# Kernel optimization log

Measured on AMD Instinct MI355X. Metric: run time of the kernel, lower is better.

The kernel has to match this reference:

```python
import jax, jax.numpy as jnp
import numpy as np

B, S, HIDDEN, H, KVH, D = 4, 1024, 4096, 32, 8, 128
ROT = D // 2  # rotary_dim = head_size/2 (inv_freq over arange(0, dim, 2))
NUM_SLOTS = 8192
ROPE_THETA = 10000.0


def setup_inputs() -> dict:
    key = jax.random.key(0)
    k0, k1, k2 = jax.random.split(key, 3)
    T = B * S
    hidden_states = jax.random.normal(k0, (T, HIDDEN), dtype=jnp.float32) * 0.02
    # RoPE tables: positions 0..S-1 per sequence, gathered per token, shape [T,1,ROT]
    inv_freq = 1.0 / (ROPE_THETA ** (np.arange(0, D, 2, dtype=np.float32) / D))
    pos = jnp.tile(jnp.arange(S, dtype=jnp.float32), B)          # [T]
    freqs = pos[:, None] * jnp.asarray(inv_freq)[None, :]        # [T, ROT]
    cos = jnp.cos(freqs)[:, None, :]
    sin = jnp.sin(freqs)[:, None, :]
    w_qkv = jax.random.normal(k1, (H * D + 2 * KVH * D, HIDDEN), dtype=jnp.float32) * 0.02
    w_o = jax.random.normal(k2, (HIDDEN, H * D), dtype=jnp.float32) * 0.02
    slots = jnp.arange(T, dtype=jnp.int32)
    key_cache = jnp.zeros((NUM_SLOTS, KVH, D), dtype=jnp.float32)
    value_cache = jnp.zeros((NUM_SLOTS, KVH, D), dtype=jnp.float32)
    return {"hidden_states": hidden_states, "cos": cos, "sin": sin,
            "w_qkv": w_qkv, "w_o": w_o,
            "key_cache": key_cache, "value_cache": value_cache,
            "slots": slots, "seq_len": S}


def _rope(x, cos, sin):
    # x: [T, heads, D]; cos/sin: [T, 1, ROT]; NeoX half-split rotation
    x1, x2 = x[..., :ROT], x[..., ROT:2 * ROT]
    return jnp.concatenate([x1 * cos - x2 * sin, x1 * sin + x2 * cos], axis=-1)


def reference(hidden_states, cos, sin, w_qkv, w_o, key_cache, value_cache, slots, seq_len):
    T, hidden = hidden_states.shape
    kvh = key_cache.shape[1]
    d = key_cache.shape[2]
    h = (w_qkv.shape[0] - 2 * kvh * d) // d
    b = T // seq_len
    groups = h // kvh
    scale = d ** -0.5

    # fused QKV projection
    qkv = hidden_states @ w_qkv.T                              # [T, (h+2*kvh)*d]
    q = qkv[:, : h * d].reshape(T, h, d)
    k = qkv[:, h * d: h * d + kvh * d].reshape(T, kvh, d)
    v = qkv[:, h * d + kvh * d:].reshape(T, kvh, d)

    # in-place RoPE on query and key
    q = _rope(q, cos, sin)
    k = _rope(k, cos, sin)

    # reshape_and_cache: scatter rotated K and V into slot-indexed cache
    new_key_cache = key_cache.at[slots].set(k)
    new_value_cache = value_cache.at[slots].set(v)

    # prefill varlen flash attention (equal-length sequences), causal, GQA
    qb = q.reshape(b, seq_len, h, d)
    kb = jnp.repeat(k.reshape(b, seq_len, kvh, d), groups, axis=2)  # [b,s,h,d]
    vb = jnp.repeat(v.reshape(b, seq_len, kvh, d), groups, axis=2)
    scores = jnp.einsum('bqhd,bkhd->bhqk', qb, kb) * scale
    causal = jnp.tril(jnp.ones((seq_len, seq_len), dtype=bool))
    scores = jnp.where(causal[None, None], scores, jnp.finfo(scores.dtype).min)
    attn = jax.nn.softmax(scores, axis=-1)
    out = jnp.einsum('bhqk,bkhd->bqhd', attn, vb).reshape(T, h * d)

    return out @ w_o.T, new_key_cache, new_value_cache
```

## Files before the change

kernel.cpp:

```cpp
#include <hip/hip_runtime.h>
#include <hip/hip_bf16.h>

#define B_    4
#define S_    1024
#define HID   4096
#define H_    32
#define KVH_  8
#define D_    128
#define T_    (B_ * S_)
#define QKVD  (H_ * D_ + 2 * KVH_ * D_)
#define NSLOT 8192

typedef __attribute__((ext_vector_type(8))) short short8;
typedef __attribute__((ext_vector_type(4))) float f32x4;

#define MFMA_B16(d, x, y) \
  d = __builtin_amdgcn_mfma_f32_16x16x32_bf16(x, y, d, 0, 0, 0)

__device__ __forceinline__ unsigned short f2b(float f) {
  union { __hip_bfloat16 h; unsigned short u; } c;
  c.h = __float2bfloat16(f);
  return c.u;
}
__device__ __forceinline__ float b2f(unsigned short u) {
  union { unsigned int i; float f; } c;
  c.i = ((unsigned int)u) << 16;
  return c.f;
}

__device__ __forceinline__ void async16(const void* g, void* l) {
  __builtin_amdgcn_global_load_lds(
      (const __attribute__((address_space(1))) unsigned int*)g,
      (__attribute__((address_space(3))) unsigned int*)l,
      16, 0, 0);
}

__global__ void conv_bf16(const float* __restrict__ src,
                          unsigned short* __restrict__ dst, int n4) {
  int i = blockIdx.x * 256 + threadIdx.x;
  if (i >= n4) return;
  float4 v = reinterpret_cast<const float4*>(src)[i];
  ushort4 o;
  o.x = f2b(v.x); o.y = f2b(v.y); o.z = f2b(v.z); o.w = f2b(v.w);
  reinterpret_cast<ushort4*>(dst)[i] = o;
}

template <bool BF16OUT>
__global__ __launch_bounds__(512, 2) void gemm_bt(
    const unsigned short* __restrict__ A, const unsigned short* __restrict__ Bm,
    void* __restrict__ Cv, int M, int N, int K) {
  __shared__ unsigned short As[2 * 2 * 128 * 64];
  __shared__ unsigned short Bs[2 * 2 * 128 * 64];
  const int tid  = threadIdx.x;
  const int lane = tid & 63;
  const int w    = tid >> 6;
  const int quad = lane >> 4;
  const int l16  = lane & 15;
  const int bm = blockIdx.y * 256;
  const int bn = blockIdx.x * 256;
  const int wmh = w >> 2;
  const int wn  = (w & 3) * 64;
  const int hB  = (w & 3) >> 1;

  const int rr  = tid >> 3;
  const int gch = ((tid & 7) ^ (rr & 7)) * 8;
  const unsigned short* gA = A + (size_t)(bm + rr) * K + gch;
  const unsigned short* gB = Bm + (size_t)(bn + rr) * K + gch;
  const size_t r64 = (size_t)64 * K;

  const int cp0 = ((quad) ^ (l16 & 7)) * 8;
  const int cp1 = ((4 + quad) ^ (l16 & 7)) * 8;
  const int abase = wmh * 8192 + l16 * 64;
  const int bbase = hB * 8192 + ((w & 1) * 64 + l16) * 64;

  f32x4 acc[8][4];
#pragma unroll
  for (int f = 0; f < 8; f++)
#pragma unroll
    for (int c = 0; c < 4; c++)
#pragma unroll
      for (int r = 0; r < 4; r++) acc[f][c][r] = 0.f;

  auto stageA = [&](int tau, int h, int buf) {
    const unsigned short* s = gA + (size_t)(h * 2) * r64 + (size_t)tau * 64;
    unsigned short* d = As + buf * 16384 + h * 8192 + tid * 8;
    async16(s, d);
    async16(s + r64, d + 4096);
  };
  auto stageB = [&](int tau, int h, int buf) {
    const unsigned short* s = gB + (size_t)(h * 2) * r64 + (size_t)tau * 64;
    unsigned short* d = Bs + buf * 16384 + h * 8192 + tid * 8;
    async16(s, d);
    async16(s + r64, d + 4096);
  };

  stageA(0, 0, 0);
  stageA(0, 1, 0);
  stageB(0, 0, 0);
  stageB(0, 1, 0);
  stageA(1, 0, 1);
  asm volatile("s_waitcnt vmcnt(2)" ::: "memory");
  __builtin_amdgcn_s_barrier();

  const int KT = K >> 6;
  short8 a[4][2], b[4][2];
  for (int t = 0; t < KT; ++t) {
    const int cb = t & 1, nb = cb ^ 1;
    const int tn1 = (t + 1 < KT) ? t + 1 : KT - 1;
    const int tn2 = (t + 2 < KT) ? t + 2 : KT - 1;
    const unsigned short* Ab = As + cb * 16384 + abase;
    const unsigned short* Bb = Bs + cb * 16384 + bbase;

#pragma unroll
    for (int f = 0; f < 4; f++) {
      a[f][0] = *(const short8*)(Ab + f * 1024 + cp0);
      a[f][1] = *(const short8*)(Ab + f * 1024 + cp1);
    }
    b[0][0] = *(const short8*)(Bb + cp0);
    b[0][1] = *(const short8*)(Bb + cp1);
    b[1][0] = *(const short8*)(Bb + 1024 + cp0);
    b[1][1] = *(const short8*)(Bb + 1024 + cp1);
    stageA(tn1, 1, nb);
    __builtin_amdgcn_s_barrier();
    __builtin_amdgcn_s_setprio(1);
#pragma unroll
    for (int f = 0; f < 4; f++) {
      MFMA_B16(acc[f][0], a[f][0], b[0][0]);
      MFMA_B16(acc[f][0], a[f][1], b[0][1]);
      MFMA_B16(acc[f][1], a[f][0], b[1][0]);
      MFMA_B16(acc[f][1], a[f][1], b[1][1]);
    }
    __builtin_amdgcn_s_setprio(0);
    __builtin_amdgcn_s_barrier();

    b[2][0] = *(const short8*)(Bb + 2048 + cp0);
    b[2][1] = *(const short8*)(Bb + 2048 + cp1);
    b[3][0] = *(const short8*)(Bb + 3072 + cp0);
    b[3][1] = *(const short8*)(Bb + 3072 + cp1);
    stageB(tn1, 0, nb);
    __builtin_amdgcn_s_barrier();
    __builtin_amdgcn_s_setprio(1);
#pragma unroll
    for (int f = 0; f < 4; f++) {
      MFMA_B16(acc[f][2], a[f][0], b[2][0]);
      MFMA_B16(acc[f][2], a[f][1], b[2][1]);
      MFMA_B16(acc[f][3], a[f][0], b[3][0]);
      MFMA_B16(acc[f][3], a[f][1], b[3][1]);
    }
    __builtin_amdgcn_s_setprio(0);
    __builtin_amdgcn_s_barrier();

#pragma unroll
    for (int f = 0; f < 4; f++) {
      a[f][0] = *(const short8*)(Ab + 4096 + f * 1024 + cp0);
      a[f][1] = *(const short8*)(Ab + 4096 + f * 1024 + cp1);
    }
    stageB(tn1, 1, nb);
    __builtin_amdgcn_s_barrier();
    __builtin_amdgcn_s_setprio(1);
#pragma unroll
    for (int f = 0; f < 4; f++) {
      MFMA_B16(acc[4 + f][0], a[f][0], b[0][0]);
      MFMA_B16(acc[4 + f][0], a[f][1], b[0][1]);
      MFMA_B16(acc[4 + f][1], a[f][0], b[1][0]);
      MFMA_B16(acc[4 + f][1], a[f][1], b[1][1]);
    }
    __builtin_amdgcn_s_setprio(0);
    __builtin_amdgcn_s_barrier();

    stageA(tn2, 0, cb);
    asm volatile("s_waitcnt vmcnt(2)" ::: "memory");
    __builtin_amdgcn_s_barrier();
    __builtin_amdgcn_s_setprio(1);
#pragma unroll
    for (int f = 0; f < 4; f++) {
      MFMA_B16(acc[4 + f][2], a[f][0], b[2][0]);
      MFMA_B16(acc[4 + f][2], a[f][1], b[2][1]);
      MFMA_B16(acc[4 + f][3], a[f][0], b[3][0]);
      MFMA_B16(acc[4 + f][3], a[f][1], b[3][1]);
    }
    __builtin_amdgcn_s_setprio(0);
    __builtin_amdgcn_s_barrier();
  }
  asm volatile("s_waitcnt vmcnt(0)" ::: "memory");

  const int crow0 = bm + wmh * 128 + quad * 4;
  const int ccol0 = bn + wn + l16;
  if constexpr (BF16OUT) {
    unsigned short* C = (unsigned short*)Cv;
#pragma unroll
    for (int f = 0; f < 8; f++)
#pragma unroll
      for (int c = 0; c < 4; c++)
#pragma unroll
        for (int r = 0; r < 4; r++)
          C[(size_t)(crow0 + f * 16 + r) * N + ccol0 + c * 16] = f2b(acc[f][c][r]);
  } else {
    float* C = (float*)Cv;
#pragma unroll
    for (int f = 0; f < 8; f++)
#pragma unroll
      for (int c = 0; c < 4; c++)
#pragma unroll
        for (int r = 0; r < 4; r++)
          C[(size_t)(crow0 + f * 16 + r) * N + ccol0 + c * 16] = acc[f][c][r];
  }
}

__global__ void rope_scatter(
    const unsigned short* __restrict__ qkv, const float* __restrict__ cosb,
    const float* __restrict__ sinb, const int* __restrict__ slots,
    unsigned short* __restrict__ qb, unsigned short* __restrict__ kb,
    unsigned short* __restrict__ vb, float* __restrict__ kco,
    float* __restrict__ vco) {
  const float sl2 = 0.08838834764831843f * 1.4426950408889634f;
  const int t = blockIdx.x;
  const int tid = threadIdx.x;
  const int b = t >> 10, s = t & 1023;
  const unsigned short* row = qkv + (size_t)t * QKVD;
  const float* cs = cosb + (size_t)t * 64;
  const float* sn = sinb + (size_t)t * 64;
  const int slot = slots[t];
  for (int wk = tid; wk < H_ * 64; wk += 256) {
    int hh = wk >> 6, i = wk & 63;
    float x1 = b2f(row[hh * D_ + i]), x2 = b2f(row[hh * D_ + 64 + i]);
    float c = cs[i], sv = sn[i];
    size_t base = ((size_t)(b * H_ + hh) * S_ + s) * D_;
    qb[base + i]      = f2b((x1 * c - x2 * sv) * sl2);
    qb[base + 64 + i] = f2b((x1 * sv + x2 * c) * sl2);
  }
  for (int wk = tid; wk < KVH_ * 64; wk += 256) {
    int hh = wk >> 6, i = wk & 63;
    float x1 = b2f(row[H_ * D_ + hh * D_ + i]);
    float x2 = b2f(row[H_ * D_ + hh * D_ + 64 + i]);
    float c = cs[i], sv = sn[i];
    float o1 = x1 * c - x2 * sv, o2 = x1 * sv + x2 * c;
    size_t base = ((size_t)(b * KVH_ + hh) * S_ + s) * D_;
    kb[base + i] = f2b(o1);
    kb[base + 64 + i] = f2b(o2);
    size_t cb = ((size_t)slot * KVH_ + hh) * D_;
    kco[cb + i] = o1;
    kco[cb + 64 + i] = o2;
  }
  for (int wk = tid; wk < KVH_ * D_; wk += 256) {
    int hh = wk >> 7, i = wk & 127;
    unsigned short xv = row[H_ * D_ + KVH_ * D_ + hh * D_ + i];
    vb[((size_t)(b * KVH_ + hh) * S_ + s) * D_ + i] = xv;
    vco[((size_t)slot * KVH_ + hh) * D_ + i] = b2f(xv);
  }
}

__global__ void transpose_v(const unsigned short* __restrict__ vb,
                            unsigned short* __restrict__ vt) {
  __shared__ unsigned short tile[64][65];
  const int bid = blockIdx.x;
  const int dt = bid & 1, st = (bid >> 1) & 15, bk = bid >> 5;
  const int tid = threadIdx.x;
  const unsigned short* src = vb + ((size_t)bk * S_ + st * 64) * D_ + dt * 64;
#pragma unroll
  for (int k = 0; k < 16; k++) {
    int e = k * 256 + tid, r = e >> 6, c = e & 63;
    tile[r][c] = src[(size_t)r * D_ + c];
  }
  __syncthreads();
  unsigned short* dst = vt + ((size_t)bk * D_ + dt * 64) * S_ + st * 64;
#pragma unroll
  for (int k = 0; k < 16; k++) {
    int e = k * 256 + tid, r = e >> 6, c = e & 63;
    dst[(size_t)r * S_ + c] = tile[c][r];
  }
}

__global__ __launch_bounds__(256) void attn_fused(
    const unsigned short* __restrict__ qb, const unsigned short* __restrict__ kb,
    const unsigned short* __restrict__ vt, unsigned short* __restrict__ ob) {
  __shared__ unsigned short Ks[4 * 64 * 32];
  __shared__ unsigned short Vs[2 * 128 * 32];
  __shared__ unsigned short Ps[4][2 * 16 * 32];
  const int tid = threadIdx.x;
  const int lane = tid & 63, w = tid >> 6;
  const int quad = lane >> 4, l16 = lane & 15;
  const int bidx = blockIdx.x;
  const int qt = 15 - (bidx & 15);
  const int bh = bidx >> 4;
  const int h = bh & 31, b = bh >> 5;
  const int kvh = h >> 2;
  const int q0 = qt * 64;
  const unsigned short* qbase = qb + ((size_t)bh * S_ + q0) * D_;
  const unsigned short* kbase = kb + (size_t)(b * KVH_ + kvh) * S_ * D_;
  const unsigned short* vbase = vt + (size_t)(b * KVH_ + kvh) * D_ * S_;

  const int srow = tid >> 2;
  const int scol = (((tid & 3) ^ ((tid >> 3) & 3)) * 8);
  const int qoff = (quad ^ ((l16 >> 1) & 3)) * 8;

#pragma unroll
  for (int i = 0; i < 4; i++)
    async16(qbase + (size_t)srow * D_ + i * 32 + scol, (unsigned short*)Ks + i * 2048 + tid * 8);
  __syncthreads();
  short8 qf[4];
#pragma unroll
  for (int kc = 0; kc < 4; kc++)
    qf[kc] = *(const short8*)(Ks + (kc * 64 + w * 16 + l16) * 32 + qoff);

  short8 of;
  {
    unsigned short ov = (l16 == 0) ? (unsigned short)0x3F80 : (unsigned short)0;
#pragma unroll
    for (int j = 0; j < 8; j++) of[j] = (short)ov;
  }

  f32x4 oac[8];
  f32x4 osum;
#pragma unroll
  for (int n = 0; n < 8; n++)
#pragma unroll
    for (int r = 0; r < 4; r++) oac[n][r] = 0.f;
#pragma unroll
  for (int r = 0; r < 4; r++) osum[r] = 0.f;
  float m_run[4] = {-3.0e38f, -3.0e38f, -3.0e38f, -3.0e38f};

  unsigned short* psw = &Ps[w][0];
  const int qrow = q0 + w * 16 + quad * 4;

  for (int jt = 0; jt <= qt; jt++) {
    __syncthreads();
    const int j0 = jt * 64;
#pragma unroll
    for (int i = 0; i < 4; i++)
      async16(kbase + (size_t)(j0 + srow) * D_ + i * 32 + scol,
              (unsigned short*)Ks + i * 2048 + tid * 8);
#pragma unroll
    for (int i = 0; i < 4; i++) {
      int kc = i >> 1;
      int d = (i & 1) * 64 + srow;
      async16(vbase + (size_t)d * S_ + j0 + kc * 32 + scol,
              (unsigned short*)Vs + i * 2048 + tid * 8);
    }
    __syncthreads();

    f32x4 sac[4];
#pragma unroll
    for (int t = 0; t < 4; t++)
#pragma unroll
      for (int r = 0; r < 4; r++) sac[t][r] = 0.f;
#pragma unroll
    for (int t = 0; t < 4; t++)
#pragma unroll
      for (int kc = 0; kc < 4; kc++)
        sac[t] = __builtin_amdgcn_mfma_f32_16x16x32_bf16(
            qf[kc], *(const short8*)(Ks + (kc * 64 + t * 16 + l16) * 32 + qoff),
            sac[t], 0, 0, 0);

    if (jt == qt) {
#pragma unroll
      for (int t = 0; t < 4; t++) {
        const int kcol = j0 + t * 16 + l16;
#pragma unroll
        for (int r = 0; r < 4; r++)
          if (kcol > qrow + r) sac[t][r] = -3.0e38f;
      }
    }
    float mx[4];
#pragma unroll
    for (int r = 0; r < 4; r++)
      mx[r] = fmaxf(fmaxf(sac[0][r], sac[1][r]), fmaxf(sac[2][r], sac[3][r]));
#pragma unroll
    for (int off = 1; off < 16; off <<= 1)
#pragma unroll
      for (int r = 0; r < 4; r++) mx[r] = fmaxf(mx[r], __shfl_xor(mx[r], off));
    float alpha[4];
#pragma unroll
    for (int r = 0; r < 4; r++) {
      float mn = fmaxf(m_run[r], mx[r]);
      alpha[r] = exp2f(m_run[r] - mn);
      m_run[r] = mn;
    }
#pragma unroll
    for (int t = 0; t < 4; t++)
#pragma unroll
      for (int r = 0; r < 4; r++) {
        float p = exp2f(sac[t][r] - m_run[r]);
        int prow = quad * 4 + r;
        int chunk = (((t & 1) * 2 + (l16 >> 3)) ^ ((prow >> 1) & 3));
        psw[(t >> 1) * 512 + prow * 32 + chunk * 8 + (l16 & 7)] = f2b(p);
      }
#pragma unroll
    for (int r = 0; r < 4; r++) osum[r] *= alpha[r];
#pragma unroll
    for (int n = 0; n < 8; n++)
#pragma unroll
      for (int r = 0; r < 4; r++) oac[n][r] *= alpha[r];
#pragma unroll
    for (int kc = 0; kc < 2; kc++) {
      short8 pf = *(const short8*)(psw + kc * 512 + l16 * 32 + qoff);
      osum = __builtin_amdgcn_mfma_f32_16x16x32_bf16(pf, of, osum, 0, 0, 0);
#pragma unroll
      for (int n = 0; n < 8; n++)
        oac[n] = __builtin_amdgcn_mfma_f32_16x16x32_bf16(
            pf, *(const short8*)(Vs + (kc * 128 + n * 16 + l16) * 32 + qoff),
            oac[n], 0, 0, 0);
    }
  }

  float inv[4];
#pragma unroll
  for (int r = 0; r < 4; r++) {
    float l = __shfl(osum[r], lane & 48, 64);
    inv[r] = 1.0f / l;
  }
  const size_t trow = (size_t)(b * S_ + q0 + w * 16 + quad * 4);
#pragma unroll
  for (int n = 0; n < 8; n++)
#pragma unroll
    for (int r = 0; r < 4; r++)
      ob[(trow + r) * (size_t)(H_ * D_) + h * D_ + n * 16 + l16] =
          f2b(oac[n][r] * inv[r]);
}

extern "C" void kernel_launch(void* const* d_in, const int* in_sizes, int n_in,
                              void* d_out, int out_size, void* d_ws, size_t ws_size,
                              hipStream_t stream) {
  const float* hidden = (const float*)d_in[0];
  const float* cosb   = (const float*)d_in[1];
  const float* sinb   = (const float*)d_in[2];
  const float* wqkv   = (const float*)d_in[3];
  const float* wo     = (const float*)d_in[4];
  const float* kc_in  = (const float*)d_in[5];
  const float* vc_in  = (const float*)d_in[6];
  const int*   slots  = (const int*)d_in[7];

  float* out    = (float*)d_out;
  float* kc_out = out + (size_t)T_ * HID;
  float* vc_out = kc_out + (size_t)NSLOT * KVH_ * D_;

  char* ws = (char*)d_ws;
  unsigned short* hb    = (unsigned short*)ws; ws += (size_t)T_ * HID * 2;
  unsigned short* wqkvb = (unsigned short*)ws; ws += (size_t)QKVD * HID * 2;
  unsigned short* wob   = (unsigned short*)ws; ws += (size_t)HID * HID * 2;
  unsigned short* qkv   = (unsigned short*)ws; ws += (size_t)T_ * QKVD * 2;
  unsigned short* qb    = (unsigned short*)ws; ws += (size_t)T_ * H_ * D_ * 2;
  unsigned short* kb    = (unsigned short*)ws; ws += (size_t)T_ * KVH_ * D_ * 2;
  unsigned short* vb    = (unsigned short*)ws; ws += (size_t)T_ * KVH_ * D_ * 2;
  unsigned short* vt    = (unsigned short*)ws; ws += (size_t)T_ * KVH_ * D_ * 2;
  unsigned short* ob    = (unsigned short*)ws;

  const size_t cache_bytes = (size_t)NSLOT * KVH_ * D_ * 4;
  hipMemcpyAsync(kc_out, kc_in, cache_bytes, hipMemcpyDeviceToDevice, stream);
  hipMemcpyAsync(vc_out, vc_in, cache_bytes, hipMemcpyDeviceToDevice, stream);

  conv_bf16<<<(T_ * HID / 4) / 256, 256, 0, stream>>>(hidden, hb, T_ * HID / 4);
  conv_bf16<<<(QKVD * HID / 4) / 256, 256, 0, stream>>>(wqkv, wqkvb, QKVD * HID / 4);
  conv_bf16<<<(HID * HID / 4) / 256, 256, 0, stream>>>(wo, wob, HID * HID / 4);

  dim3 g1(QKVD / 256, T_ / 256);
  gemm_bt<true><<<g1, 512, 0, stream>>>(hb, wqkvb, qkv, T_, QKVD, HID);

  rope_scatter<<<T_, 256, 0, stream>>>(qkv, cosb, sinb, slots, qb, kb, vb, kc_out, vc_out);

  transpose_v<<<B_ * KVH_ * 16 * 2, 256, 0, stream>>>(vb, vt);

  attn_fused<<<B_ * H_ * (S_ / 64), 256, 0, stream>>>(qb, kb, vt, ob);

  dim3 g2(HID / 256, T_ / 256);
  gemm_bt<false><<<g2, 512, 0, stream>>>(ob, wob, out, T_, HID, HID);
}
```

Before: 918.4 us.

## Add a 256x192-tile QKV GEMM kernel to balance the grid across CUs

Adds a dedicated bf16 GEMM kernel for the QKV projection with 256x192 output tiles in place of 256x256. With N=6144 this gives 512 blocks, matching two resident blocks on each of 256 CUs, where the old tiling gave 384 blocks and left slots idle. The kernel has its own double-buffered async LDS pipeline with interleaved MFMA phases and priority hints. The trade-off is less operand reuse per tile, and the epilogue still writes scalar bf16 values with strided addresses.

```diff
diff --git a/kernel.cpp b/kernel.cpp
--- a/kernel.cpp
+++ b/kernel.cpp
@@ -43,6 +43,162 @@
   ushort4 o;
   o.x = f2b(v.x); o.y = f2b(v.y); o.z = f2b(v.z); o.w = f2b(v.w);
   reinterpret_cast<ushort4*>(dst)[i] = o;
+}
+
+__global__ __launch_bounds__(512, 2) void gemm1_192(
+    const unsigned short* __restrict__ A, const unsigned short* __restrict__ Bm,
+    unsigned short* __restrict__ C, int M, int N, int K) {
+  __shared__ unsigned short As[2 * 16384];
+  __shared__ unsigned short Bs[2 * 12288];
+  const int tid  = threadIdx.x;
+  const int lane = tid & 63;
+  const int w    = tid >> 6;
+  const int quad = lane >> 4;
+  const int l16  = lane & 15;
+  const int bm = blockIdx.y * 256;
+  const int bn = blockIdx.x * 192;
+  const int wmh = w >> 2;
+  const int wn  = (w & 3) * 48;
+
+  const int rr  = tid >> 3;
+  const int gch = ((tid & 7) ^ (rr & 7)) * 8;
+  const unsigned short* gA = A + (size_t)(bm + rr) * K + gch;
+  const unsigned short* gB = Bm + (size_t)(bn + rr) * K + gch;
+  const size_t r64 = (size_t)64 * K;
+
+  const int cp0 = ((quad) ^ (l16 & 7)) * 8;
+  const int cp1 = ((4 + quad) ^ (l16 & 7)) * 8;
+  const int abase = wmh * 8192 + l16 * 64;
+  const int bbase = (wn + l16) * 64;
+
+  f32x4 acc[8][3];
+#pragma unroll
+  for (int f = 0; f < 8; f++)
+#pragma unroll
+    for (int c = 0; c < 3; c++)
+#pragma unroll
+      for (int r = 0; r < 4; r++) acc[f][c][r] = 0.f;
+
+  auto stA = [&](int tau, int h, int buf) {
+    const unsigned short* s = gA + (size_t)(h * 2) * r64 + (size_t)tau * 64;
+    unsigned short* d = As + buf * 16384 + h * 8192 + tid * 8;
+    async16(s, d);
+    async16(s + r64, d + 4096);
+  };
+  auto stB = [&](int tau, int g, int buf) {
+    const unsigned short* s = gB + (size_t)g * r64 + (size_t)tau * 64;
+    unsigned short* d = Bs + buf * 12288 + g * 4096 + tid * 8;
+    async16(s, d);
+  };
+
+  stA(0, 0, 0);
+  stA(0, 1, 0);
+  stB(0, 0, 0); stB(0, 1, 0); stB(0, 2, 0);
+  stA(1, 0, 1);
+  asm volatile("s_waitcnt vmcnt(2)" ::: "memory");
+  __builtin_amdgcn_s_barrier();
+
+  short8 aA[4][2], aB[4][2], b[3][2];
+  {
+    const unsigned short* Ab = As + abase;
+    const unsigned short* Bb = Bs + bbase;
+#pragma unroll
+    for (int f = 0; f < 4; f++) {
+      aA[f][0] = *(const short8*)(Ab + f * 1024 + cp0);
+      aA[f][1] = *(const short8*)(Ab + f * 1024 + cp1);
+    }
+    b[0][0] = *(const short8*)(Bb + cp0);
+    b[0][1] = *(const short8*)(Bb + cp1);
+    b[1][0] = *(const short8*)(Bb + 1024 + cp0);
+    b[1][1] = *(const short8*)(Bb + 1024 + cp1);
+  }
+
+  const int KT = K >> 6;
+  for (int t = 0; t < KT; ++t) {
+    const int cb = t & 1, nb = cb ^ 1;
+    const int tn1 = (t + 1 < KT) ? t + 1 : KT - 1;
+    const int tn2 = (t + 2 < KT) ? t + 2 : KT - 1;
+    const unsigned short* Ab  = As + cb * 16384 + abase;
+    const unsigned short* Bb  = Bs + cb * 12288 + bbase;
+    const unsigned short* Abn = As + nb * 16384 + abase;
+    const unsigned short* Bbn = Bs + nb * 12288 + bbase;
+
+    stA(tn1, 1, nb);
+    __builtin_amdgcn_s_barrier();
+    b[2][0] = *(const short8*)(Bb + 2048 + cp0);
+    b[2][1] = *(const short8*)(Bb + 2048 + cp1);
+    __builtin_amdgcn_s_setprio(1);
+#pragma unroll
+    for (int f = 0; f < 4; f++) {
+      MFMA_B16(acc[f][0], aA[f][0], b[0][0]);
+      MFMA_B16(acc[f][0], aA[f][1], b[0][1]);
+      MFMA_B16(acc[f][1], aA[f][0], b[1][0]);
+      MFMA_B16(acc[f][1], aA[f][1], b[1][1]);
+    }
+    __builtin_amdgcn_s_setprio(0);
+    __builtin_amdgcn_s_barrier();
+
+    stB(tn1, 0, nb); stB(tn1, 1, nb);
+    __builtin_amdgcn_s_barrier();
+#pragma unroll
+    for (int f = 0; f < 4; f++) {
+      aB[f][0] = *(const short8*)(Ab + 4096 + f * 1024 + cp0);
+      aB[f][1] = *(const short8*)(Ab + 4096 + f * 1024 + cp1);
+    }
+    __builtin_amdgcn_s_setprio(1);
+#pragma unroll
+    for (int f = 0; f < 4; f++) {
+      MFMA_B16(acc[f][2], aA[f][0], b[2][0]);
+      MFMA_B16(acc[f][2], aA[f][1], b[2][1]);
+    }
+    __builtin_amdgcn_s_setprio(0);
+    __builtin_amdgcn_s_barrier();
+
+    stB(tn1, 2, nb);
+    __builtin_amdgcn_s_barrier();
+    __builtin_amdgcn_s_setprio(1);
+#pragma unroll
+    for (int f = 0; f < 4; f++) {
+      MFMA_B16(acc[4 + f][0], aB[f][0], b[0][0]);
+      MFMA_B16(acc[4 + f][0], aB[f][1], b[0][1]);
+      MFMA_B16(acc[4 + f][1], aB[f][0], b[1][0]);
+      MFMA_B16(acc[4 + f][1], aB[f][1], b[1][1]);
+    }
+    __builtin_amdgcn_s_setprio(0);
+    __builtin_amdgcn_s_barrier();
+
+    stA(tn2, 0, cb);
+    asm volatile("s_waitcnt vmcnt(2)" ::: "memory");
+    __builtin_amdgcn_s_barrier();
+#pragma unroll
+    for (int f = 0; f < 4; f++) {
+      aA[f][0] = *(const short8*)(Abn + f * 1024 + cp0);
+      aA[f][1] = *(const short8*)(Abn + f * 1024 + cp1);
+    }
+    b[0][0] = *(const short8*)(Bbn + cp0);
+    b[0][1] = *(const short8*)(Bbn + cp1);
+    b[1][0] = *(const short8*)(Bbn + 1024 + cp0);
+    b[1][1] = *(const short8*)(Bbn + 1024 + cp1);
+    __builtin_amdgcn_s_setprio(1);
+#pragma unroll
+    for (int f = 0; f < 4; f++) {
+      MFMA_B16(acc[4 + f][2], aB[f][0], b[2][0]);
+      MFMA_B16(acc[4 + f][2], aB[f][1], b[2][1]);
+    }
+    __builtin_amdgcn_s_setprio(0);
+    __builtin_amdgcn_s_barrier();
+  }
+  asm volatile("s_waitcnt vmcnt(0)" ::: "memory");
+
+  const int crow0 = bm + wmh * 128 + quad * 4;
+  const int ccol0 = bn + wn + l16;
+#pragma unroll
+  for (int f = 0; f < 8; f++)
+#pragma unroll
+    for (int c = 0; c < 3; c++)
+#pragma unroll
+      for (int r = 0; r < 4; r++)
+        C[(size_t)(crow0 + f * 16 + r) * N + ccol0 + c * 16] = f2b(acc[f][c][r]);
 }
 
 template <bool BF16OUT>
@@ -453,8 +609,8 @@
   conv_bf16<<<(QKVD * HID / 4) / 256, 256, 0, stream>>>(wqkv, wqkvb, QKVD * HID / 4);
   conv_bf16<<<(HID * HID / 4) / 256, 256, 0, stream>>>(wo, wob, HID * HID / 4);
 
-  dim3 g1(QKVD / 256, T_ / 256);
-  gemm_bt<true><<<g1, 512, 0, stream>>>(hb, wqkvb, qkv, T_, QKVD, HID);
+  dim3 g1(QKVD / 192, T_ / 256);
+  gemm1_192<<<g1, 512, 0, stream>>>(hb, wqkvb, qkv, T_, QKVD, HID);
 
   rope_scatter<<<T_, 256, 0, stream>>>(qkv, cosb, sinb, slots, qb, kb, vb, kc_out, vc_out);
 
```

Measured after the change: 960.0 us. +4.5%, slower.
